# Kernel tuning notes

Hardware: AMD Instinct MI355X
Metric: run time of the kernel (lower is better)

The kernel has to match this reference:

```python
import jax, jax.numpy as jnp
import numpy as np

NEG_SLOPE = 0.2  # PyG GATConv default leaky_relu slope
N_NODES, IN_DIM, HID, HEADS, OUT = 50000, 128, 64, 4, 128
N_EDGES = 800000


def gat_conv(x, src, dst, num_nodes, W, a_src, a_dst, bias, concat):
    """One PyG-style GATConv (add_self_loops already applied to src/dst)."""
    H, C = a_src.shape
    xp = (x @ W).reshape(num_nodes, H, C)            # (N,H,C)
    s = jnp.einsum('nhc,hc->nh', xp, a_src)          # per-node src score
    d = jnp.einsum('nhc,hc->nh', xp, a_dst)          # per-node dst score
    e = s[src] + d[dst]                              # (E,H)
    e = jnp.where(e > 0, e, NEG_SLOPE * e)           # leaky_relu
    # segment softmax over edges grouped by destination node
    m = jax.ops.segment_max(e, dst, num_segments=num_nodes)
    p = jnp.exp(e - m[dst])
    z = jax.ops.segment_sum(p, dst, num_segments=num_nodes)
    alpha = p / (z[dst] + 1e-16)                     # (E,H)
    # scatter-aggregate messages
    out = jax.ops.segment_sum(xp[src] * alpha[:, :, None], dst, num_segments=num_nodes)
    out = out.reshape(num_nodes, H * C) if concat else out.mean(axis=1)
    return out + bias


def setup_inputs() -> dict:
    key = jax.random.key(0)
    ks = jax.random.split(key, 16)
    HC = HEADS * HID
    inp = {
        'x': jax.random.normal(ks[0], (N_NODES, IN_DIM), dtype=jnp.float32),
        'edge_index': jax.random.randint(ks[1], (2, N_EDGES), 0, N_NODES, dtype=jnp.int32),
        'W0': jax.random.normal(ks[2], (IN_DIM, HC), dtype=jnp.float32) * 0.08,
        'a_src0': jax.random.normal(ks[3], (HEADS, HID), dtype=jnp.float32) * 0.1,
        'a_dst0': jax.random.normal(ks[4], (HEADS, HID), dtype=jnp.float32) * 0.1,
        'b0': jnp.zeros((HC,), dtype=jnp.float32),
        'W1': jax.random.normal(ks[5], (HC, HC), dtype=jnp.float32) * 0.06,
        'a_src1': jax.random.normal(ks[6], (HEADS, HID), dtype=jnp.float32) * 0.1,
        'a_dst1': jax.random.normal(ks[7], (HEADS, HID), dtype=jnp.float32) * 0.1,
        'b1': jnp.zeros((HC,), dtype=jnp.float32),
        'W2': jax.random.normal(ks[8], (HC, OUT), dtype=jnp.float32) * 0.06,
        'a_src2': jax.random.normal(ks[9], (1, OUT), dtype=jnp.float32) * 0.1,
        'a_dst2': jax.random.normal(ks[10], (1, OUT), dtype=jnp.float32) * 0.1,
        'b2': jnp.zeros((OUT,), dtype=jnp.float32),
    }
    return inp


def reference(x, edge_index, W0, a_src0, a_dst0, b0, W1, a_src1, a_dst1, b1, W2, a_src2, a_dst2, b2):
    N = x.shape[0]
    loops = jnp.arange(N, dtype=edge_index.dtype)  # add_self_loops=True
    src = jnp.concatenate([edge_index[0], loops])
    dst = jnp.concatenate([edge_index[1], loops])
    h = gat_conv(x, src, dst, N, W0, a_src0, a_dst0, b0, True)
    h = jax.nn.elu(h)
    h = gat_conv(h, src, dst, N, W1, a_src1, a_dst1, b1, True)
    h = jax.nn.elu(h)
    h = gat_conv(h, src, dst, N, W2, a_src2, a_dst2, b2, False)
    return h
```

## Files before the change

kernel.cpp:

```cpp
#include <hip/hip_runtime.h>
#include <hip/hip_bf16.h>
#include <hip/hip_fp16.h>
#include <math.h>

#define N_NODES 50000
#define N_EDGES 800000
#define ET      (N_EDGES + N_NODES)
#define IN_DIM  128
#define HEADS   4
#define HID     64
#define HC      256
#define OUTD    128

typedef _Float16 half8 __attribute__((ext_vector_type(8)));
typedef float f32x4 __attribute__((ext_vector_type(4)));


__global__ void scan1_k(const int* __restrict__ counts, int* __restrict__ offs,
                        int* __restrict__ bsums) {
    __shared__ int sm[512];
    int tid = threadIdx.x;
    int i = blockIdx.x * 512 + tid;
    int v = (i < N_NODES) ? counts[i] : 0;
    sm[tid] = v;
    __syncthreads();
    #pragma unroll
    for (int o = 1; o < 512; o <<= 1) {
        int add = (tid >= o) ? sm[tid - o] : 0;
        __syncthreads();
        sm[tid] += add;
        __syncthreads();
    }
    if (i < N_NODES) offs[i] = sm[tid] - v;
    if (tid == 511) bsums[blockIdx.x] = sm[511];
}

__global__ void scan2_k(int* __restrict__ bsums, int nb) {
    __shared__ int sm[128];
    int tid = threadIdx.x;
    int v = (tid < nb) ? bsums[tid] : 0;
    sm[tid] = v;
    __syncthreads();
    #pragma unroll
    for (int o = 1; o < 128; o <<= 1) {
        int add = (tid >= o) ? sm[tid - o] : 0;
        __syncthreads();
        sm[tid] += add;
        __syncthreads();
    }
    if (tid < nb) bsums[tid] = sm[tid] - v;
}

__global__ void scan3_k(int* __restrict__ offs, const int* __restrict__ bsums) {
    int i = blockIdx.x * 512 + threadIdx.x;
    if (i < N_NODES) offs[i] += bsums[blockIdx.x];
    if (i == 0) offs[N_NODES] = ET;
}

__global__ void fill_k(const int* __restrict__ ei, const int* __restrict__ offs,
                       int* __restrict__ counts, int* __restrict__ csr) {
    int i = blockIdx.x * blockDim.x + threadIdx.x;
    if (i >= ET) return;
    int sv, dv;
    if (i < N_EDGES) { sv = ei[i]; dv = ei[N_EDGES + i]; }
    else             { sv = dv = i - N_EDGES; }
    int pos = offs[dv] + atomicSub(&counts[dv], 1) - 1;
    csr[pos] = sv;
}


#define J_HIST  ET
#define J_CVT   (N_NODES * IN_DIM / 4)
#define J_W     131072
#define SETUP_TOTAL (J_HIST + J_CVT + J_W + 2 * N_NODES)

__global__ void setup_k(const int* __restrict__ ei, int* __restrict__ counts,
                        const float* __restrict__ x, __half* __restrict__ xh,
                        const float* __restrict__ W0, __half* __restrict__ Wt0,
                        const float* __restrict__ W1, __half* __restrict__ Wt1,
                        const float* __restrict__ W2, __half* __restrict__ Wt2,
                        float* __restrict__ S2, float* __restrict__ D2) {
    int g = blockIdx.x * 256 + threadIdx.x;
    if (g < J_HIST) {
        int dv = (g < N_EDGES) ? ei[N_EDGES + g] : (g - N_EDGES);
        atomicAdd(&counts[dv], 1);
        return;
    }
    g -= J_HIST;
    if (g < J_CVT) {
        float4 v = *(const float4*)(x + (size_t)g * 4);
        union { __half2 h2[2]; float2 f2; } u;
        u.h2[0] = __floats2half2_rn(v.x, v.y);
        u.h2[1] = __floats2half2_rn(v.z, v.w);
        *(float2*)(xh + (size_t)g * 4) = u.f2;
        return;
    }
    g -= J_CVT;
    if (g < J_W) {
        if (g < 32768) {
            int n = g / IN_DIM, k = g - n * IN_DIM;
            Wt0[g] = __float2half(W0[(size_t)k * HC + n]);
        } else if (g < 98304) {
            int i = g - 32768;
            int n = i / HC, k = i - n * HC;
            Wt1[i] = __float2half(W1[(size_t)k * HC + n]);
        } else {
            int i = g - 98304;
            int n = i / HC, k = i - n * HC;
            Wt2[i] = __float2half(W2[(size_t)k * OUTD + n]);
        }
        return;
    }
    g -= J_W;
    if (g < N_NODES) { S2[g] = 0.f; return; }
    g -= N_NODES;
    if (g < N_NODES) D2[g] = 0.f;
}


__device__ __forceinline__ void async_copy16(void* lds_base, const void* gaddr) {
    __builtin_amdgcn_global_load_lds(
        (const __attribute__((address_space(1))) unsigned int*)gaddr,
        (__attribute__((address_space(3))) unsigned int*)lds_base,
        16, 0, 0);
}

#define CPAD 132

template<int H, int CD, bool ATOMIC>
__global__ __launch_bounds__(256) void gemm_mfma_k(const __half* __restrict__ A,
                                                   const __half* __restrict__ Wt,
                                                   __half* __restrict__ C,
                                                   const float* __restrict__ asrc,
                                                   const float* __restrict__ adst,
                                                   float* __restrict__ S,
                                                   float* __restrict__ D,
                                                   int M, int K, int N) {
    __shared__ __attribute__((aligned(16))) __half smem[128 * CPAD];
    __half* Ah = smem;
    __half* Bh = smem + 128 * 64;
    const int t = threadIdx.x;
    const int w = t >> 6;
    const int lane = t & 63;
    const int wm = w >> 1, wn = w & 1;
    const int cc = lane & 15;
    const int quad = lane >> 4;
    const int row0 = blockIdx.x * 128;
    const int col0 = blockIdx.y * 128;

    f32x4 acc[4][4];
    #pragma unroll
    for (int i = 0; i < 4; ++i)
        #pragma unroll
        for (int j = 0; j < 4; ++j) acc[i][j] = (f32x4){0.f, 0.f, 0.f, 0.f};

    const int srow = lane >> 3;
    const int skq  = (lane & 7) * 8;

    for (int k0 = 0; k0 < K; k0 += 64) {
        __syncthreads();
        #pragma unroll
        for (int hh = 0; hh < 4; ++hh) {
            int ra = row0 + w * 32 + hh * 8 + srow;
            if (ra > M - 1) ra = M - 1;
            async_copy16(&Ah[(w * 32 + hh * 8) * 64],
                         A + (size_t)ra * K + k0 + skq);
            int rb = col0 + w * 32 + hh * 8 + srow;
            async_copy16(&Bh[(w * 32 + hh * 8) * 64],
                         Wt + (size_t)rb * K + k0 + skq);
        }
        __syncthreads();
        #pragma unroll
        for (int c = 0; c < 2; ++c) {
            half8 a[4], b[4];
            #pragma unroll
            for (int i = 0; i < 4; ++i)
                a[i] = *(const half8*)&Ah[(wm * 64 + i * 16 + cc) * 64 + c * 32 + quad * 8];
            #pragma unroll
            for (int j = 0; j < 4; ++j)
                b[j] = *(const half8*)&Bh[(wn * 64 + j * 16 + cc) * 64 + c * 32 + quad * 8];
            #pragma unroll
            for (int i = 0; i < 4; ++i)
                #pragma unroll
                for (int j = 0; j < 4; ++j)
                    acc[i][j] = __builtin_amdgcn_mfma_f32_16x16x32_f16(b[j], a[i], acc[i][j], 0, 0, 0);
        }
    }

    const int hh_ = ATOMIC ? 0 : (blockIdx.y * 2 + wn);
    float4 asj[4], adj[4];
    #pragma unroll
    for (int j = 0; j < 4; ++j) {
        int cb = (ATOMIC ? wn * 64 : 0) + j * 16 + quad * 4;
        asj[j] = *(const float4*)&asrc[hh_ * CD + cb];
        adj[j] = *(const float4*)&adst[hh_ * CD + cb];
    }
    #pragma unroll
    for (int i = 0; i < 4; ++i) {
        float sv = 0.f, dv = 0.f;
        #pragma unroll
        for (int j = 0; j < 4; ++j) {
            sv = fmaf(acc[i][j][0], asj[j].x, sv); dv = fmaf(acc[i][j][0], adj[j].x, dv);
            sv = fmaf(acc[i][j][1], asj[j].y, sv); dv = fmaf(acc[i][j][1], adj[j].y, dv);
            sv = fmaf(acc[i][j][2], asj[j].z, sv); dv = fmaf(acc[i][j][2], adj[j].z, dv);
            sv = fmaf(acc[i][j][3], asj[j].w, sv); dv = fmaf(acc[i][j][3], adj[j].w, dv);
        }
        sv += __shfl_xor(sv, 16, 64); dv += __shfl_xor(dv, 16, 64);
        sv += __shfl_xor(sv, 32, 64); dv += __shfl_xor(dv, 32, 64);
        int r = row0 + wm * 64 + i * 16 + cc;
        if (quad == 0 && r < M) {
            if constexpr (ATOMIC) {
                atomicAdd(&S[r], sv);
                atomicAdd(&D[r], dv);
            } else {
                S[(size_t)r * H + hh_] = sv;
                D[(size_t)r * H + hh_] = dv;
            }
        }
    }

    __syncthreads();
    #pragma unroll
    for (int i = 0; i < 4; ++i) {
        int tr = wm * 64 + i * 16 + cc;
        #pragma unroll
        for (int j = 0; j < 4; ++j) {
            int tc = wn * 64 + j * 16 + quad * 4;
            union { __half2 h2[2]; uint2 u2; } pk;
            pk.h2[0] = __floats2half2_rn(acc[i][j][0], acc[i][j][1]);
            pk.h2[1] = __floats2half2_rn(acc[i][j][2], acc[i][j][3]);
            *(uint2*)&smem[tr * CPAD + tc] = pk.u2;
        }
    }
    __syncthreads();
    #pragma unroll
    for (int rr = 0; rr < 8; ++rr) {
        int r = rr * 16 + (t >> 4);
        int ccol = (t & 15) * 8;
        uint4 v = *(const uint4*)&smem[r * CPAD + ccol];
        int gr = row0 + r;
        if (gr < M)
            *(uint4*)&C[(size_t)gr * N + col0 + ccol] = v;
    }
}


template<int H, int C, bool ELU_OUT, typename OT>
__global__ __launch_bounds__(256) void aggr_k(const __half* __restrict__ xp,
                                              const float* __restrict__ s,
                                              const float* __restrict__ d,
                                              const int* __restrict__ offs,
                                              const int* __restrict__ csr,
                                              const float* __restrict__ bias,
                                              OT* __restrict__ out) {
    constexpr int HCl = H * C;
    constexpr int EPL = HCl / 64;
    constexpr int U = 8;
    int wid = blockIdx.x * 4 + (threadIdx.x >> 6);
    int lane = threadIdx.x & 63;
    if (wid >= N_NODES) return;
    int h = (lane * EPL) / C;
    float dh = d[(size_t)wid * H + h];
    float z = 0.f;
    float acc[EPL];
    #pragma unroll
    for (int k = 0; k < EPL; ++k) acc[k] = 0.f;

    auto loadrow = [&](int src, float* v) {
        const __half* xr = xp + (size_t)src * HCl + lane * EPL;
        if constexpr (EPL == 4) {
            union { float2 f2; __half2 h2[2]; } u;
            u.f2 = *(const float2*)xr;
            float2 a = __half22float2(u.h2[0]);
            float2 b = __half22float2(u.h2[1]);
            v[0] = a.x; v[1] = a.y; v[2] = b.x; v[3] = b.y;
        } else {
            union { float f; __half2 h2; } u;
            u.f = *(const float*)xr;
            float2 a = __half22float2(u.h2);
            v[0] = a.x; v[1] = a.y;
        }
    };

    int e0 = offs[wid], e1 = offs[wid + 1];
    int j = e0;
    for (; j + U <= e1; j += U) {
        int srcs[U];
        #pragma unroll
        for (int u = 0; u < U; ++u) srcs[u] = csr[j + u];
        float ev[U];
        #pragma unroll
        for (int u = 0; u < U; ++u) ev[u] = s[(size_t)srcs[u] * H + h];
        float v[U][EPL];
        #pragma unroll
        for (int u = 0; u < U; ++u) loadrow(srcs[u], v[u]);
        #pragma unroll
        for (int u = 0; u < U; ++u) {
            float e = ev[u] + dh;
            e = (e > 0.f) ? e : 0.2f * e;
            float p = __expf(e);
            z += p;
            #pragma unroll
            for (int k = 0; k < EPL; ++k) acc[k] += p * v[u][k];
        }
    }
    for (; j < e1; ++j) {
        int sv = csr[j];
        float e = s[(size_t)sv * H + h] + dh;
        e = (e > 0.f) ? e : 0.2f * e;
        float p = __expf(e);
        float v[EPL];
        loadrow(sv, v);
        z += p;
        #pragma unroll
        for (int k = 0; k < EPL; ++k) acc[k] += p * v[k];
    }

    float inv = 1.f / (z + 1e-16f);
    float o[EPL];
    #pragma unroll
    for (int k = 0; k < EPL; ++k) {
        o[k] = acc[k] * inv + bias[lane * EPL + k];
        if constexpr (ELU_OUT) o[k] = (o[k] > 0.f) ? o[k] : (__expf(o[k]) - 1.f);
    }
    if constexpr (sizeof(OT) == 2 && EPL == 4) {
        union { __half2 h2[2]; float2 f2; } u;
        u.h2[0] = __floats2half2_rn(o[0], o[1]);
        u.h2[1] = __floats2half2_rn(o[2], o[3]);
        *(float2*)((__half*)out + (size_t)wid * HCl + lane * EPL) = u.f2;
    } else {
        #pragma unroll
        for (int k = 0; k < EPL; ++k)
            out[(size_t)wid * HCl + lane * EPL + k] = (OT)o[k];
    }
}


extern "C" void kernel_launch(void* const* d_in, const int* in_sizes, int n_in,
                              void* d_out, int out_size, void* d_ws, size_t ws_size,
                              hipStream_t stream) {
    const float* x      = (const float*)d_in[0];
    const int*   ei     = (const int*)  d_in[1];
    const float* W0     = (const float*)d_in[2];
    const float* as0    = (const float*)d_in[3];
    const float* ad0    = (const float*)d_in[4];
    const float* b0     = (const float*)d_in[5];
    const float* W1     = (const float*)d_in[6];
    const float* as1    = (const float*)d_in[7];
    const float* ad1    = (const float*)d_in[8];
    const float* b1     = (const float*)d_in[9];
    const float* W2     = (const float*)d_in[10];
    const float* as2    = (const float*)d_in[11];
    const float* ad2    = (const float*)d_in[12];
    const float* b2     = (const float*)d_in[13];
    float* out = (float*)d_out;

    char* p = (char*)d_ws;
    auto take = [&](size_t bytes) {
        char* r = p;
        p += (bytes + 255) & ~(size_t)255;
        return r;
    };
    __half* XPh   = (__half*)take((size_t)N_NODES * HC * 2);
    __half* Hbuf  = (__half*)take((size_t)N_NODES * HC * 2);
    __half* xh    = (__half*)take((size_t)N_NODES * IN_DIM * 2);
    __half* Wt0   = (__half*)take((size_t)IN_DIM * HC * 2);
    __half* Wt1   = (__half*)take((size_t)HC * HC * 2);
    __half* Wt2   = (__half*)take((size_t)HC * OUTD * 2);
    float*  S     = (float*) take((size_t)N_NODES * HEADS * 4);
    float*  D     = (float*) take((size_t)N_NODES * HEADS * 4);
    float*  S2    = (float*) take((size_t)N_NODES * 4);
    float*  D2    = (float*) take((size_t)N_NODES * 4);
    int*    counts= (int*)   take((size_t)N_NODES * 4);
    int*    offs  = (int*)   take((size_t)(N_NODES + 1) * 4);
    int*    bsums = (int*)   take(512 * 4);
    int*    csr   = (int*)   take((size_t)ET * 4);

    const int NB_SCAN = (N_NODES + 511) / 512;
    const int ET_BLOCKS = (ET + 255) / 256;
    const int NODE_BLOCKS = (N_NODES + 3) / 4;

    hipMemsetAsync(counts, 0, (size_t)N_NODES * 4, stream);
    setup_k<<<(SETUP_TOTAL + 255) / 256, 256, 0, stream>>>(
        ei, counts, x, xh, W0, Wt0, W1, Wt1, W2, Wt2, S2, D2);

    scan1_k<<<NB_SCAN, 512, 0, stream>>>(counts, offs, bsums);
    scan2_k<<<1, 128, 0, stream>>>(bsums, NB_SCAN);
    scan3_k<<<NB_SCAN, 512, 0, stream>>>(offs, bsums);
    fill_k<<<ET_BLOCKS, 256, 0, stream>>>(ei, offs, counts, csr);

    const int MB = (N_NODES + 127) / 128;
    dim3 g0(MB, HC / 128);
    dim3 g2(MB, OUTD / 128);

    gemm_mfma_k<HEADS, HID, false><<<g0, 256, 0, stream>>>(xh, Wt0, XPh, as0, ad0, S, D, N_NODES, IN_DIM, HC);
    aggr_k<HEADS, HID, true, __half><<<NODE_BLOCKS, 256, 0, stream>>>(XPh, S, D, offs, csr, b0, Hbuf);

    gemm_mfma_k<HEADS, HID, false><<<g0, 256, 0, stream>>>(Hbuf, Wt1, XPh, as1, ad1, S, D, N_NODES, HC, HC);
    aggr_k<HEADS, HID, true, __half><<<NODE_BLOCKS, 256, 0, stream>>>(XPh, S, D, offs, csr, b1, Hbuf);

    gemm_mfma_k<1, OUTD, true><<<g2, 256, 0, stream>>>(Hbuf, Wt2, XPh, as2, ad2, S2, D2, N_NODES, HC, OUTD);
    aggr_k<1, OUTD, false, float><<<NODE_BLOCKS, 256, 0, stream>>>(XPh, S2, D2, offs, csr, b2, out);
}
```

Before: 412.9 us.

## Merge three-pass scan into one kernel and double GEMM K-tile to 128

Replaces the three-kernel prefix scan over node degrees with a single 1024-thread block. Each thread scans a contiguous chunk, which removes two launches and the block-sums buffer. The GEMM now stages a 128-wide K slice per iteration instead of 64, halving the number of barrier-separated load/compute rounds. The cost is doubling LDS to 64KB per block, which may lower occupancy. The single-block scan also serialises about 49 elements per thread with strided, uncoalesced loads.

```diff
diff --git a/kernel.cpp b/kernel.cpp
--- a/kernel.cpp
+++ b/kernel.cpp
@@ -16,45 +16,32 @@
 typedef float f32x4 __attribute__((ext_vector_type(4)));
 
 
-__global__ void scan1_k(const int* __restrict__ counts, int* __restrict__ offs,
-                        int* __restrict__ bsums) {
-    __shared__ int sm[512];
-    int tid = threadIdx.x;
-    int i = blockIdx.x * 512 + tid;
-    int v = (i < N_NODES) ? counts[i] : 0;
-    sm[tid] = v;
+__global__ __launch_bounds__(1024) void scan_all_k(const int* __restrict__ counts,
+                                                   int* __restrict__ offs) {
+    __shared__ int sm[1024];
+    constexpr int T = 1024;
+    constexpr int CH = (N_NODES + T - 1) / T;
+    const int t = threadIdx.x;
+    const int base = t * CH;
+    int s = 0;
+    for (int i = 0; i < CH; ++i) {
+        int idx = base + i;
+        if (idx < N_NODES) s += counts[idx];
+    }
+    sm[t] = s;
     __syncthreads();
-    #pragma unroll
-    for (int o = 1; o < 512; o <<= 1) {
-        int add = (tid >= o) ? sm[tid - o] : 0;
+    for (int o = 1; o < T; o <<= 1) {
+        int add = (t >= o) ? sm[t - o] : 0;
         __syncthreads();
-        sm[tid] += add;
+        sm[t] += add;
         __syncthreads();
     }
-    if (i < N_NODES) offs[i] = sm[tid] - v;
-    if (tid == 511) bsums[blockIdx.x] = sm[511];
-}
-
-__global__ void scan2_k(int* __restrict__ bsums, int nb) {
-    __shared__ int sm[128];
-    int tid = threadIdx.x;
-    int v = (tid < nb) ? bsums[tid] : 0;
-    sm[tid] = v;
-    __syncthreads();
-    #pragma unroll
-    for (int o = 1; o < 128; o <<= 1) {
-        int add = (tid >= o) ? sm[tid - o] : 0;
-        __syncthreads();
-        sm[tid] += add;
-        __syncthreads();
-    }
-    if (tid < nb) bsums[tid] = sm[tid] - v;
-}
-
-__global__ void scan3_k(int* __restrict__ offs, const int* __restrict__ bsums) {
-    int i = blockIdx.x * 512 + threadIdx.x;
-    if (i < N_NODES) offs[i] += bsums[blockIdx.x];
-    if (i == 0) offs[N_NODES] = ET;
+    int run = sm[t] - s;
+    for (int i = 0; i < CH; ++i) {
+        int idx = base + i;
+        if (idx < N_NODES) { offs[idx] = run; run += counts[idx]; }
+    }
+    if (t == 0) offs[N_NODES] = ET;
 }
 
 __global__ void fill_k(const int* __restrict__ ei, const int* __restrict__ offs,
@@ -136,9 +123,9 @@
                                                    float* __restrict__ S,
                                                    float* __restrict__ D,
                                                    int M, int K, int N) {
-    __shared__ __attribute__((aligned(16))) __half smem[128 * CPAD];
+    __shared__ __attribute__((aligned(16))) __half smem[2 * 128 * 128];
     __half* Ah = smem;
-    __half* Bh = smem + 128 * 64;
+    __half* Bh = smem + 128 * 128;
     const int t = threadIdx.x;
     const int w = t >> 6;
     const int lane = t & 63;
@@ -154,31 +141,31 @@
         #pragma unroll
         for (int j = 0; j < 4; ++j) acc[i][j] = (f32x4){0.f, 0.f, 0.f, 0.f};
 
-    const int srow = lane >> 3;
-    const int skq  = (lane & 7) * 8;
-
-    for (int k0 = 0; k0 < K; k0 += 64) {
+    const int srow = lane >> 4;
+    const int skq  = (lane & 15) * 8;
+
+    for (int k0 = 0; k0 < K; k0 += 128) {
         __syncthreads();
         #pragma unroll
-        for (int hh = 0; hh < 4; ++hh) {
-            int ra = row0 + w * 32 + hh * 8 + srow;
+        for (int hh = 0; hh < 8; ++hh) {
+            int ra = row0 + w * 32 + hh * 4 + srow;
             if (ra > M - 1) ra = M - 1;
-            async_copy16(&Ah[(w * 32 + hh * 8) * 64],
+            async_copy16(&Ah[(w * 32 + hh * 4) * 128],
                          A + (size_t)ra * K + k0 + skq);
-            int rb = col0 + w * 32 + hh * 8 + srow;
-            async_copy16(&Bh[(w * 32 + hh * 8) * 64],
+            int rb = col0 + w * 32 + hh * 4 + srow;
+            async_copy16(&Bh[(w * 32 + hh * 4) * 128],
                          Wt + (size_t)rb * K + k0 + skq);
         }
         __syncthreads();
         #pragma unroll
-        for (int c = 0; c < 2; ++c) {
+        for (int c = 0; c < 4; ++c) {
             half8 a[4], b[4];
             #pragma unroll
             for (int i = 0; i < 4; ++i)
-                a[i] = *(const half8*)&Ah[(wm * 64 + i * 16 + cc) * 64 + c * 32 + quad * 8];
+                a[i] = *(const half8*)&Ah[(wm * 64 + i * 16 + cc) * 128 + c * 32 + quad * 8];
             #pragma unroll
             for (int j = 0; j < 4; ++j)
-                b[j] = *(const half8*)&Bh[(wn * 64 + j * 16 + cc) * 64 + c * 32 + quad * 8];
+                b[j] = *(const half8*)&Bh[(wn * 64 + j * 16 + cc) * 128 + c * 32 + quad * 8];
             #pragma unroll
             for (int i = 0; i < 4; ++i)
                 #pragma unroll
@@ -237,10 +224,11 @@
     for (int rr = 0; rr < 8; ++rr) {
         int r = rr * 16 + (t >> 4);
         int ccol = (t & 15) * 8;
-        uint4 v = *(const uint4*)&smem[r * CPAD + ccol];
         int gr = row0 + r;
-        if (gr < M)
+        if (gr < M) {
+            uint4 v = *(const uint4*)&smem[r * CPAD + ccol];
             *(uint4*)&C[(size_t)gr * N + col0 + ccol] = v;
+        }
     }
 }
 
@@ -373,25 +361,20 @@
     float*  D2    = (float*) take((size_t)N_NODES * 4);
     int*    counts= (int*)   take((size_t)N_NODES * 4);
     int*    offs  = (int*)   take((size_t)(N_NODES + 1) * 4);
-    int*    bsums = (int*)   take(512 * 4);
     int*    csr   = (int*)   take((size_t)ET * 4);
 
-    const int NB_SCAN = (N_NODES + 511) / 512;
     const int ET_BLOCKS = (ET + 255) / 256;
     const int NODE_BLOCKS = (N_NODES + 3) / 4;
+    const int MB = (N_NODES + 127) / 128;
+    dim3 g0(MB, HC / 128);
+    dim3 g2(MB, OUTD / 128);
 
     hipMemsetAsync(counts, 0, (size_t)N_NODES * 4, stream);
     setup_k<<<(SETUP_TOTAL + 255) / 256, 256, 0, stream>>>(
         ei, counts, x, xh, W0, Wt0, W1, Wt1, W2, Wt2, S2, D2);
 
-    scan1_k<<<NB_SCAN, 512, 0, stream>>>(counts, offs, bsums);
-    scan2_k<<<1, 128, 0, stream>>>(bsums, NB_SCAN);
-    scan3_k<<<NB_SCAN, 512, 0, stream>>>(offs, bsums);
+    scan_all_k<<<1, 1024, 0, stream>>>(counts, offs);
     fill_k<<<ET_BLOCKS, 256, 0, stream>>>(ei, offs, counts, csr);
-
-    const int MB = (N_NODES + 127) / 128;
-    dim3 g0(MB, HC / 128);
-    dim3 g2(MB, OUTD / 128);
 
     gemm_mfma_k<HEADS, HID, false><<<g0, 256, 0, stream>>>(xh, Wt0, XPh, as0, ad0, S, D, N_NODES, IN_DIM, HC);
     aggr_k<HEADS, HID, true, __half><<<NODE_BLOCKS, 256, 0, stream>>>(XPh, S, D, offs, csr, b0, Hbuf);
```

Measured after the change: 508.3 us. +23.1%, slower.
